# Kernel optimization log

Hardware: AMD Instinct MI355X
Metric: run time of the kernel (lower is better)

## Reference

```python
import jax, jax.numpy as jnp
import numpy as np

N = 100000   # nodes
E = 1600000  # edges (avg degree 16)
G = 1024     # graphs in batch
F = 128      # node feature dim
H = 128      # hidden channels


def setup_inputs() -> dict:
    key = jax.random.key(0)
    ks = jax.random.split(key, 12)
    s = 1.0 / np.sqrt(H)
    x = jax.random.normal(ks[0], (N, F), dtype=jnp.float32)
    edge_index = jax.random.randint(ks[1], (2, E), 0, N, dtype=jnp.int32)
    batch = jnp.sort(jax.random.randint(ks[2], (N,), 0, G, dtype=jnp.int32))
    return {
        "x": x,
        "edge_index": edge_index,
        "batch": batch,
        "W1": jax.random.normal(ks[3], (F, H), dtype=jnp.float32) * s,
        "b1": jnp.zeros((H,), jnp.float32),
        "W2": jax.random.normal(ks[4], (H, H), dtype=jnp.float32) * s,
        "b2": jnp.zeros((H,), jnp.float32),
        "W3": jax.random.normal(ks[5], (H, H), dtype=jnp.float32) * s,
        "b3": jnp.zeros((H,), jnp.float32),
        "W4": jax.random.normal(ks[6], (H, H), dtype=jnp.float32) * s,
        "b4": jnp.zeros((H,), jnp.float32),
        "linW": jax.random.normal(ks[7], (H, 2), dtype=jnp.float32) * s,
        "linb": jnp.zeros((2,), jnp.float32),
    }


def _gcn_conv(h, W, b, src, dst, norm, n):
    # h' = D^{-1/2}(A+I)D^{-1/2} (h W) + b   (PyG GCNConv default)
    m = h @ W                              # [n, H]
    msg = m[src] * norm[:, None]           # [E+n, H] gather + scale
    out = jax.ops.segment_sum(msg, dst, num_segments=n)
    return out + b


def reference(x, edge_index, batch, W1, b1, W2, b2, W3, b3, W4, b4, linW, linb):
    n = x.shape[0]
    loops = jnp.arange(n, dtype=edge_index.dtype)
    src = jnp.concatenate([edge_index[0], loops])   # add self-loops
    dst = jnp.concatenate([edge_index[1], loops])
    deg = jax.ops.segment_sum(jnp.ones_like(dst, dtype=x.dtype), dst, num_segments=n)
    dinv = jax.lax.rsqrt(deg)                       # deg >= 1 due to self-loops
    norm = dinv[src] * dinv[dst]                    # [E+n]

    h = jax.nn.relu(_gcn_conv(x, W1, b1, src, dst, norm, n))
    h = jax.nn.relu(_gcn_conv(h, W2, b2, src, dst, norm, n))
    h = jax.nn.relu(_gcn_conv(h, W3, b3, src, dst, norm, n))
    h = jax.nn.relu(_gcn_conv(h, W4, b4, src, dst, norm, n))

    # global_mean_pool over `batch` segment ids
    counts = jax.ops.segment_sum(jnp.ones((n,), x.dtype), batch, num_segments=G)
    pooled = jax.ops.segment_sum(h, batch, num_segments=G) / jnp.maximum(counts, 1.0)[:, None]

    # dropout p=0.5 is identity in eval mode
    return pooled @ linW + linb
```

## Files before the change

kernel.cpp:

```cpp
#include <hip/hip_runtime.h>
#include <math.h>

#define NF 128
#define NU 64
#define NQ 32
#define TROWS 32
#define ARS 68
#define CRS 132
#define QS  16.0f
#define QIS 0.0625f

#define SRC_BITS 18
#define SRC_MASK ((1u << SRC_BITS) - 1u)
#define BCS 32
#define EPB 2048

typedef unsigned int  u32;
typedef unsigned short u16;
typedef u32 b4 __attribute__((ext_vector_type(2)));
typedef short bf16x8 __attribute__((ext_vector_type(8)));
typedef float f32x4 __attribute__((ext_vector_type(4)));
typedef float f32x2 __attribute__((ext_vector_type(2)));

__device__ inline u16 f2bf(float f) {
    u32 u = __float_as_uint(f);
    return (u16)((u + 0x7fffu + ((u >> 16) & 1u)) >> 16);
}
__device__ inline u32 pack2(float a, float b) {
    return (u32)f2bf(a) | ((u32)f2bf(b) << 16);
}
__device__ inline float bflo(u32 u) { return __uint_as_float(u << 16); }
__device__ inline float bfhi(u32 u) { return __uint_as_float(u & 0xffff0000u); }

__device__ inline u32 pack4(float a, float b, float c, float d) {
    u32 v = __builtin_amdgcn_cvt_pk_fp8_f32(a, b, 0, false);
    v = __builtin_amdgcn_cvt_pk_fp8_f32(c, d, v, true);
    return v;
}
__device__ inline void acc4(float4& a, u32 q) {
    f32x2 lo = __builtin_amdgcn_cvt_pk_f32_fp8(q, false);
    f32x2 hi = __builtin_amdgcn_cvt_pk_f32_fp8(q, true);
    a.x += lo[0]; a.y += lo[1]; a.z += hi[0]; a.w += hi[1];
}


__global__ __launch_bounds__(256) void k_bscat(const int* __restrict__ ei,
                                               int* bcur, u32* __restrict__ pairs,
                                               int E, int bshift, int cap) {
    __shared__ int h[256];
    __shared__ int rb[256];
    int t = threadIdx.x;
    h[t] = 0;
    __syncthreads();
    int base = blockIdx.x * EPB;
    #pragma unroll
    for (int k = 0; k < EPB / 256; ++k) {
        int e = base + k * 256 + t;
        if (e < E) atomicAdd(&h[ei[E + e] >> bshift], 1);
    }
    __syncthreads();
    int c = h[t];
    if (c) rb[t] = t * cap + atomicAdd(&bcur[t * BCS], c);
    h[t] = 0;
    __syncthreads();
    #pragma unroll
    for (int k = 0; k < EPB / 256; ++k) {
        int e = base + k * 256 + t;
        if (e < E) {
            int d = ei[E + e];
            int b = d >> bshift;
            int p = rb[b] + atomicAdd(&h[b], 1);
            u32 rel = (u32)(d - (b << bshift));
            pairs[p] = (rel << SRC_BITS) | (u32)ei[e];
        }
    }
}

__global__ __launch_bounds__(512) void k_degscan(const u32* __restrict__ pairs,
        const int* __restrict__ bcur, float* __restrict__ dinv,
        int* __restrict__ offs, int* __restrict__ bsum,
        int n, int bshift, int cap) {
    extern __shared__ int sh[];
    int bsz = 1 << bshift;
    int* deg = sh;
    int* ss = sh + bsz;
    int b = blockIdx.x, b0 = b << bshift, t = threadIdx.x;
    for (int i = t; i < bsz; i += 512) deg[i] = 0;
    __syncthreads();
    int lo = b * cap, hi = lo + bcur[b * BCS];
    for (int j = lo + t; j < hi; j += 512)
        atomicAdd(&deg[pairs[j] >> SRC_BITS], 1);
    __syncthreads();
    int C = bsz >> 9;
    int vloc[8];
    int tsum = 0;
    for (int c = 0; c < C; ++c) {
        int i = t * C + c;
        int node = b0 + i;
        int v = 0;
        if (node < n) {
            int real = deg[i] + 1;
            dinv[node] = 1.0f / sqrtf((float)real);
            v = (real + 3) & ~3;
        }
        vloc[c] = tsum;
        tsum += v;
    }
    ss[t] = tsum;
    for (int d = 1; d < 512; d <<= 1) {
        __syncthreads();
        int a = (t >= d) ? ss[t - d] : 0;
        __syncthreads();
        ss[t] += a;
    }
    __syncthreads();
    int tbase = ss[t] - tsum;
    for (int c = 0; c < C; ++c) {
        int node = b0 + t * C + c;
        if (node < n) offs[node] = tbase + vloc[c];
    }
    if (t == 511) bsum[b] = ss[511];
}

__global__ __launch_bounds__(512) void k_csr(const u32* __restrict__ pairs,
        const int* __restrict__ bcur, const int* __restrict__ bsum,
        int* __restrict__ offs, int* __restrict__ srcS,
        int n, int nbk, int bshift, int cap) {
    extern __shared__ int sh[];
    __shared__ int ss[512];
    int bsz = 1 << bshift;
    int* cur = sh;
    int* endv = sh + bsz;
    int b = blockIdx.x, b0 = b << bshift, t = threadIdx.x;

    int v = (t < nbk) ? bsum[t] : 0;
    ss[t] = v;
    for (int d = 1; d < 512; d <<= 1) {
        __syncthreads();
        int a = (t >= d) ? ss[t - d] : 0;
        __syncthreads();
        ss[t] += a;
    }
    __syncthreads();
    int bsumb = bsum[b];
    int base = ss[b] - bsumb;
    int nextbase = ss[b];
    int total = ss[511];
    if (b == nbk - 1 && t == 0) offs[n] = total;

    for (int i = t; i < bsz; i += 512) {
        int node = b0 + i;
        int o = 0;
        if (node < n) {
            o = offs[node] + base;
            offs[node] = o;
        }
        cur[i] = o;
    }
    __syncthreads();
    for (int i = t; i < bsz; i += 512) {
        int node = b0 + i;
        int e;
        if (node + 1 >= n)       e = total;
        else if (i < bsz - 1)    e = cur[i + 1];
        else                     e = nextbase;
        endv[i] = e;
    }
    __syncthreads();
    int lo = b * cap, hi = lo + bcur[b * BCS];
    for (int j = lo + t; j < hi; j += 512) {
        u32 vv = pairs[j];
        int p = atomicAdd(&cur[vv >> SRC_BITS], 1);
        srcS[p] = (int)(vv & SRC_MASK);
    }
    __syncthreads();
    for (int i = t; i < bsz; i += 512) {
        int node = b0 + i;
        if (node < n) {
            int c = cur[i];
            srcS[c] = node;
            int e = endv[i];
            for (int k = c + 1; k < e; ++k) srcS[k] = n;
        }
    }
}

__global__ __launch_bounds__(256) void k_pack(const float* __restrict__ x,
                       const float* __restrict__ dinv, u32* __restrict__ q,
                       const float* __restrict__ W0, const float* __restrict__ W1,
                       const float* __restrict__ W2, const float* __restrict__ W3,
                       u32* __restrict__ wt, int n) {
    int t = blockIdx.x * blockDim.x + threadIdx.x;
    int totalu4 = (n + 1) * (NQ / 4);
    if (t < totalu4) {
        int row = t >> 3;
        uint4 o = make_uint4(0, 0, 0, 0);
        if (row < n) {
            int cbase = (t & 7) << 4;
            const float* xr = x + (size_t)row * NF + cbase;
            f32x4 f0 = __builtin_nontemporal_load((const f32x4*)(xr));
            f32x4 f1 = __builtin_nontemporal_load((const f32x4*)(xr + 4));
            f32x4 f2 = __builtin_nontemporal_load((const f32x4*)(xr + 8));
            f32x4 f3 = __builtin_nontemporal_load((const f32x4*)(xr + 12));
            float d = dinv[row] * QS;
            o.x = pack4(f0.x * d, f0.y * d, f0.z * d, f0.w * d);
            o.y = pack4(f1.x * d, f1.y * d, f1.z * d, f1.w * d);
            o.z = pack4(f2.x * d, f2.y * d, f2.z * d, f2.w * d);
            o.w = pack4(f3.x * d, f3.y * d, f3.z * d, f3.w * d);
        }
        ((uint4*)q)[t] = o;
    }
    if (t < 4 * 2048) {
        int layer = t >> 11;
        int rem = t & 2047;
        int lane = rem & 63;
        int ks = (rem >> 6) & 3;
        int nt = rem >> 8;
        const float* W = layer == 0 ? W0 : layer == 1 ? W1 : layer == 2 ? W2 : W3;
        int nn = nt * 16 + (lane & 15);
        int k0 = ks * 32 + (lane >> 4) * 8;
        uint4 o;
        o.x = pack2(W[(k0 + 0) * NF + nn], W[(k0 + 1) * NF + nn]);
        o.y = pack2(W[(k0 + 2) * NF + nn], W[(k0 + 3) * NF + nn]);
        o.z = pack2(W[(k0 + 4) * NF + nn], W[(k0 + 5) * NF + nn]);
        o.w = pack2(W[(k0 + 6) * NF + nn], W[(k0 + 7) * NF + nn]);
        ((uint4*)wt)[t] = o;
    }
}

__global__ __launch_bounds__(256, 8) void k_fused(
        const u32* __restrict__ hin, const int* __restrict__ offs,
        const int* __restrict__ srcS, const float* __restrict__ dinv,
        const u32* __restrict__ wt, const float* __restrict__ bias,
        u32* __restrict__ out, int* tctr, int n, int ntiles, int last) {
    __shared__ __align__(16) u32 buf[TROWS * CRS];
    __shared__ int stile;
    float* Cs = (float*)buf;
    int tid = threadIdx.x;
    int grp = tid >> 5;
    int lane32 = tid & 31;
    int c4 = lane32 << 2;
    int cu = lane32 << 1;
    int cq = lane32;
    int wv = tid >> 6;
    int lane = tid & 63;
    int m0 = (wv & 1) * 16;
    int nh = wv >> 1;
    int mrow = lane & 15, quad = lane >> 4;

    float4 bv = *(const float4*)(bias + c4);

    for (;;) {
        if (tid == 0) stile = atomicAdd(tctr, 1);
        __syncthreads();
        int tile = stile;
        if (tile >= ntiles) break;
        int row0 = tile * TROWS;

        #pragma unroll
        for (int i = 0; i < 4; ++i) {
            int r = grp * 4 + i;
            int node = row0 + r;
            float4 acc = make_float4(0.f, 0.f, 0.f, 0.f);
            if (node < n) {
                int b = offs[node], e = offs[node + 1];
                int j = b;
                for (; j + 8 <= e; j += 8) {
                    int4 sa = *(const int4*)(srcS + j);
                    int4 sb = *(const int4*)(srcS + j + 4);
                    u32 q0 = hin[(size_t)sa.x * NQ + cq];
                    u32 q1 = hin[(size_t)sa.y * NQ + cq];
                    u32 q2 = hin[(size_t)sa.z * NQ + cq];
                    u32 q3 = hin[(size_t)sa.w * NQ + cq];
                    u32 q4 = hin[(size_t)sb.x * NQ + cq];
                    u32 q5 = hin[(size_t)sb.y * NQ + cq];
                    u32 q6 = hin[(size_t)sb.z * NQ + cq];
                    u32 q7 = hin[(size_t)sb.w * NQ + cq];
                    acc4(acc, q0); acc4(acc, q1); acc4(acc, q2); acc4(acc, q3);
                    acc4(acc, q4); acc4(acc, q5); acc4(acc, q6); acc4(acc, q7);
                }
                if (j < e) {
                    int4 sa = *(const int4*)(srcS + j);
                    u32 q0 = hin[(size_t)sa.x * NQ + cq];
                    u32 q1 = hin[(size_t)sa.y * NQ + cq];
                    u32 q2 = hin[(size_t)sa.z * NQ + cq];
                    u32 q3 = hin[(size_t)sa.w * NQ + cq];
                    acc4(acc, q0); acc4(acc, q1); acc4(acc, q2); acc4(acc, q3);
                }
                float dn = dinv[node];
                acc.x *= dn; acc.y *= dn; acc.z *= dn; acc.w *= dn;
            }
            b4 o; o.x = pack2(acc.x, acc.y); o.y = pack2(acc.z, acc.w);
            *(b4*)(buf + r * ARS + cu) = o;
        }
        __syncthreads();

        f32x4 a0 = {0.f, 0.f, 0.f, 0.f}, a1 = a0, a2 = a0, a3 = a0;
        #pragma unroll
        for (int ks = 0; ks < 4; ++ks) {
            bf16x8 a = *(const bf16x8*)(buf + (m0 + mrow) * ARS + ks * 16 + quad * 4);
            const u32* wb = wt + (((nh * 4) * 4 + ks) * 64 + lane) * 4;
            bf16x8 b0 = *(const bf16x8*)(wb);
            bf16x8 b1 = *(const bf16x8*)(wb + 1024);
            bf16x8 b2 = *(const bf16x8*)(wb + 2048);
            bf16x8 b3 = *(const bf16x8*)(wb + 3072);
            a0 = __builtin_amdgcn_mfma_f32_16x16x32_bf16(a, b0, a0, 0, 0, 0);
            a1 = __builtin_amdgcn_mfma_f32_16x16x32_bf16(a, b1, a1, 0, 0, 0);
            a2 = __builtin_amdgcn_mfma_f32_16x16x32_bf16(a, b2, a2, 0, 0, 0);
            a3 = __builtin_amdgcn_mfma_f32_16x16x32_bf16(a, b3, a3, 0, 0, 0);
        }
        __syncthreads();

        #pragma unroll
        for (int nt = 0; nt < 4; ++nt) {
            f32x4 av = nt == 0 ? a0 : nt == 1 ? a1 : nt == 2 ? a2 : a3;
            int col = (nh * 4 + nt) * 16 + mrow;
            #pragma unroll
            for (int rg = 0; rg < 4; ++rg)
                Cs[(m0 + quad * 4 + rg) * CRS + col] = av[rg];
        }
        __syncthreads();

        #pragma unroll
        for (int j = 0; j < 4; ++j) {
            int r = grp * 4 + j;
            int gr = row0 + r;
            if (gr <= n) {
                if (last) {
                    b4 o; o.x = 0u; o.y = 0u;
                    if (gr < n) {
                        float4 v = *(const float4*)(Cs + r * CRS + c4);
                        float ox = fmaxf(v.x * QIS + bv.x, 0.f);
                        float oy = fmaxf(v.y * QIS + bv.y, 0.f);
                        float oz = fmaxf(v.z * QIS + bv.z, 0.f);
                        float ow = fmaxf(v.w * QIS + bv.w, 0.f);
                        o.x = pack2(ox, oy);
                        o.y = pack2(oz, ow);
                    }
                    *(b4*)(out + (size_t)gr * NU + cu) = o;
                } else {
                    u32 o = 0u;
                    if (gr < n) {
                        float4 v = *(const float4*)(Cs + r * CRS + c4);
                        float sc = dinv[gr] * QS;
                        float ox = fmaxf(v.x * QIS + bv.x, 0.f) * sc;
                        float oy = fmaxf(v.y * QIS + bv.y, 0.f) * sc;
                        float oz = fmaxf(v.z * QIS + bv.z, 0.f) * sc;
                        float ow = fmaxf(v.w * QIS + bv.w, 0.f) * sc;
                        o = pack4(ox, oy, oz, ow);
                    }
                    out[(size_t)gr * NQ + cq] = o;
                }
            }
        }
        __syncthreads();
    }
}


__global__ __launch_bounds__(256) void k_poolfinal(const u32* __restrict__ h,
        const int* __restrict__ batch, const float* __restrict__ linW,
        const float* __restrict__ linb, float* __restrict__ outp, int N) {
    int g = blockIdx.x;
    int tid = threadIdx.x;
    __shared__ int sb[2];
    if (tid < 2) {
        int target = g + tid;
        int lo = 0, hi = N;
        while (lo < hi) {
            int mid = (lo + hi) >> 1;
            if (batch[mid] < target) lo = mid + 1; else hi = mid;
        }
        sb[tid] = lo;
    }
    __syncthreads();
    int b = sb[0], e = sb[1];

    int grp = tid >> 5, lane = tid & 31;
    int c4 = lane << 2, cu = lane << 1;
    float4 acc = make_float4(0.f, 0.f, 0.f, 0.f);
    for (int i = b + grp; i < e; i += 8) {
        b4 v = *(const b4*)(h + (size_t)i * NU + cu);
        acc.x += bflo(v.x); acc.y += bfhi(v.x);
        acc.z += bflo(v.y); acc.w += bfhi(v.y);
    }
    __shared__ float red[8][NF];
    *(float4*)(&red[grp][c4]) = acc;
    __syncthreads();

    float v0 = 0.f, v1 = 0.f;
    if (tid < NF) {
        float s = 0.f;
        #pragma unroll
        for (int gg = 0; gg < 8; ++gg) s += red[gg][tid];
        v0 = s * linW[tid * 2 + 0];
        v1 = s * linW[tid * 2 + 1];
    }
    #pragma unroll
    for (int d = 32; d > 0; d >>= 1) {
        v0 += __shfl_down(v0, d);
        v1 += __shfl_down(v1, d);
    }
    __shared__ float sv[8];
    if ((tid & 63) == 0) { sv[(tid >> 6) * 2] = v0; sv[(tid >> 6) * 2 + 1] = v1; }
    __syncthreads();
    if (tid == 0) {
        float inv = 1.0f / fmaxf((float)(e - b), 1.0f);
        outp[g * 2 + 0] = (sv[0] + sv[2]) * inv + linb[0];
        outp[g * 2 + 1] = (sv[1] + sv[3]) * inv + linb[1];
    }
}


extern "C" void kernel_launch(void* const* d_in, const int* in_sizes, int n_in,
                              void* d_out, int out_size, void* d_ws, size_t ws_size,
                              hipStream_t stream) {
    const float* x     = (const float*)d_in[0];
    const int*   ei    = (const int*)d_in[1];
    const int*   batch = (const int*)d_in[2];
    const float* Wl[4] = {(const float*)d_in[3], (const float*)d_in[5],
                          (const float*)d_in[7], (const float*)d_in[9]};
    const float* bl[4] = {(const float*)d_in[4], (const float*)d_in[6],
                          (const float*)d_in[8], (const float*)d_in[10]};
    const float* linW  = (const float*)d_in[11];
    const float* linb  = (const float*)d_in[12];
    float* out = (float*)d_out;

    const int N  = in_sizes[2];
    const int E  = in_sizes[1] / 2;
    const int G  = out_size / 2;

    int bshift = 9;
    while (((N + (1 << bshift) - 1) >> bshift) > 256) ++bshift;
    int nbk = (N + (1 << bshift) - 1) >> bshift;
    int bsz = 1 << bshift;
    int cap = ((E / nbk) * 5 / 4 + 1024 + 255) & ~255;

    char* p = (char*)d_ws;
    auto carve = [&](size_t bytes) -> char* {
        char* r = p;
        p += (bytes + 255) & ~(size_t)255;
        return r;
    };
    float* dinv   = (float*)carve((size_t)N * 4);
    int*   offs   = (int*)  carve((size_t)(N + 1) * 4);
    int*   bsum   = (int*)  carve(512 * 4);
    int*   bcur   = (int*)  carve(256 * BCS * 4);
    int*   tctr   = (int*)  carve(4 * 4);
    u32*   wt     = (u32*)  carve(4 * 2048 * 16);
    int*   srcS   = (int*)  carve((size_t)(E + 4 * (size_t)N) * 4);
    u32*   bufA   = (u32*)  carve((size_t)(N + 1) * NU * 4);
    u32*   bufB   = (u32*)  carve((size_t)(N + 1) * NU * 4);
    u32*   pairs  = bufB;

    size_t zbytes = (char*)(tctr + 4) - (char*)bcur;
    (void)hipMemsetAsync(bcur, 0, zbytes, stream);

    int nblkE = (E + EPB - 1) / EPB;
    k_bscat<<<nblkE, 256, 0, stream>>>(ei, bcur, pairs, E, bshift, cap);
    k_degscan<<<nbk, 512, (bsz + 512) * 4, stream>>>(pairs, bcur, dinv, offs,
                                                     bsum, N, bshift, cap);
    k_csr<<<nbk, 512, 2 * bsz * 4, stream>>>(pairs, bcur, bsum, offs, srcS,
                                             N, nbk, bshift, cap);

    int totalu4 = (N + 1) * (NQ / 4);
    int packT = totalu4 > 8192 ? totalu4 : 8192;
    k_pack<<<(packT + 255) / 256, 256, 0, stream>>>(x, dinv, bufA,
                                                    Wl[0], Wl[1], Wl[2], Wl[3], wt, N);

    int ntiles = (N + 1 + TROWS - 1) / TROWS;
    int ngrid = ntiles < 2048 ? ntiles : 2048;
    const u32* hin = bufA;
    u32* hout = bufB;
    for (int l = 0; l < 4; ++l) {
        k_fused<<<ngrid, 256, 0, stream>>>(hin, offs, srcS, dinv, wt + l * 8192,
                                           bl[l], hout, tctr + l, N, ntiles, l == 3);
        hin = hout;
        hout = (hout == bufA) ? bufB : bufA;
    }

    k_poolfinal<<<G, 256, 0, stream>>>(hin, batch, linW, linb, out, N);
}
```

Baseline: 538.0 us.

## Partition each node's CSR neighbors into four source-range slices for gather locality

Each destination node's neighbor list is split into four segments by source-node range, each padded to a multiple of four. The fused layer kernel walks all tiles' nodes slice by slice, with a block barrier between slices, so concurrent blocks gather from a narrower part of the feature array and hit cache more often. The cost is extra padding entries (up to four pads per node), a bigger offset table, more shared memory and work in the CSR build, and extra barriers in the gather loop.

```diff
diff --git a/kernel.cpp b/kernel.cpp
--- a/kernel.cpp
+++ b/kernel.cpp
@@ -14,6 +14,7 @@
 #define SRC_MASK ((1u << SRC_BITS) - 1u)
 #define BCS 32
 #define EPB 2048
+#define NSL 4
 
 typedef unsigned int  u32;
 typedef unsigned short u16;
@@ -78,33 +79,42 @@
 
 __global__ __launch_bounds__(512) void k_degscan(const u32* __restrict__ pairs,
         const int* __restrict__ bcur, float* __restrict__ dinv,
-        int* __restrict__ offs, int* __restrict__ bsum,
-        int n, int bshift, int cap) {
+        int* __restrict__ offs, int* __restrict__ offsS4, int* __restrict__ bsum,
+        int n, int bshift, int cap, int slw) {
     extern __shared__ int sh[];
     int bsz = 1 << bshift;
     int* deg = sh;
-    int* ss = sh + bsz;
+    int* ss = sh + bsz * 4;
     int b = blockIdx.x, b0 = b << bshift, t = threadIdx.x;
-    for (int i = t; i < bsz; i += 512) deg[i] = 0;
+    for (int i = t; i < bsz * 4; i += 512) deg[i] = 0;
     __syncthreads();
     int lo = b * cap, hi = lo + bcur[b * BCS];
-    for (int j = lo + t; j < hi; j += 512)
-        atomicAdd(&deg[pairs[j] >> SRC_BITS], 1);
+    for (int j = lo + t; j < hi; j += 512) {
+        u32 v = pairs[j];
+        int rel = v >> SRC_BITS;
+        int src = (int)(v & SRC_MASK);
+        int s = src / slw; if (s > 3) s = 3;
+        atomicAdd(&deg[rel * 4 + s], 1);
+    }
     __syncthreads();
     int C = bsz >> 9;
-    int vloc[8];
+    int vst[8];
     int tsum = 0;
     for (int c = 0; c < C; ++c) {
         int i = t * C + c;
         int node = b0 + i;
-        int v = 0;
+        vst[c] = tsum;
         if (node < n) {
-            int real = deg[i] + 1;
+            int ssl = node / slw; if (ssl > 3) ssl = 3;
+            int real = 1;
+            #pragma unroll
+            for (int s = 0; s < 4; ++s) {
+                int cc = deg[i * 4 + s] + (s == ssl ? 1 : 0);
+                real += deg[i * 4 + s];
+                tsum += (cc + 3) & ~3;
+            }
             dinv[node] = 1.0f / sqrtf((float)real);
-            v = (real + 3) & ~3;
-        }
-        vloc[c] = tsum;
-        tsum += v;
+        }
     }
     ss[t] = tsum;
     for (int d = 1; d < 512; d <<= 1) {
@@ -116,21 +126,32 @@
     __syncthreads();
     int tbase = ss[t] - tsum;
     for (int c = 0; c < C; ++c) {
-        int node = b0 + t * C + c;
-        if (node < n) offs[node] = tbase + vloc[c];
+        int i = t * C + c;
+        int node = b0 + i;
+        if (node < n) {
+            int pos = tbase + vst[c];
+            offs[node] = pos;
+            int ssl = node / slw; if (ssl > 3) ssl = 3;
+            #pragma unroll
+            for (int s = 0; s < 4; ++s) {
+                offsS4[node * 4 + s] = pos;
+                int cc = deg[i * 4 + s] + (s == ssl ? 1 : 0);
+                pos += (cc + 3) & ~3;
+            }
+        }
     }
     if (t == 511) bsum[b] = ss[511];
 }
 
 __global__ __launch_bounds__(512) void k_csr(const u32* __restrict__ pairs,
         const int* __restrict__ bcur, const int* __restrict__ bsum,
-        int* __restrict__ offs, int* __restrict__ srcS,
-        int n, int nbk, int bshift, int cap) {
+        int* __restrict__ offs, int* __restrict__ offsS4, int* __restrict__ srcS,
+        int n, int nbk, int bshift, int cap, int slw) {
     extern __shared__ int sh[];
     __shared__ int ss[512];
     int bsz = 1 << bshift;
     int* cur = sh;
-    int* endv = sh + bsz;
+    int* endv = sh + bsz * 4;
     int b = blockIdx.x, b0 = b << bshift, t = threadIdx.x;
 
     int v = (t < nbk) ? bsum[t] : 0;
@@ -142,45 +163,62 @@
         ss[t] += a;
     }
     __syncthreads();
-    int bsumb = bsum[b];
-    int base = ss[b] - bsumb;
+    int base = ss[b] - bsum[b];
     int nextbase = ss[b];
     int total = ss[511];
     if (b == nbk - 1 && t == 0) offs[n] = total;
 
     for (int i = t; i < bsz; i += 512) {
         int node = b0 + i;
-        int o = 0;
         if (node < n) {
-            o = offs[node] + base;
-            offs[node] = o;
-        }
-        cur[i] = o;
+            offs[node] += base;
+            int4 o4 = *(int4*)(offsS4 + node * 4);
+            o4.x += base; o4.y += base; o4.z += base; o4.w += base;
+            *(int4*)(offsS4 + node * 4) = o4;
+            cur[i * 4 + 0] = o4.x; cur[i * 4 + 1] = o4.y;
+            cur[i * 4 + 2] = o4.z; cur[i * 4 + 3] = o4.w;
+        } else {
+            cur[i * 4 + 0] = 0; cur[i * 4 + 1] = 0;
+            cur[i * 4 + 2] = 0; cur[i * 4 + 3] = 0;
+        }
     }
     __syncthreads();
     for (int i = t; i < bsz; i += 512) {
         int node = b0 + i;
-        int e;
-        if (node + 1 >= n)       e = total;
-        else if (i < bsz - 1)    e = cur[i + 1];
-        else                     e = nextbase;
-        endv[i] = e;
+        if (node < n) {
+            endv[i * 4 + 0] = cur[i * 4 + 1];
+            endv[i * 4 + 1] = cur[i * 4 + 2];
+            endv[i * 4 + 2] = cur[i * 4 + 3];
+            int e3;
+            if (node + 1 >= n)    e3 = total;
+            else if (i < bsz - 1) e3 = cur[(i + 1) * 4 + 0];
+            else                  e3 = nextbase;
+            endv[i * 4 + 3] = e3;
+        }
     }
     __syncthreads();
     int lo = b * cap, hi = lo + bcur[b * BCS];
     for (int j = lo + t; j < hi; j += 512) {
         u32 vv = pairs[j];
-        int p = atomicAdd(&cur[vv >> SRC_BITS], 1);
-        srcS[p] = (int)(vv & SRC_MASK);
+        int rel = vv >> SRC_BITS;
+        int src = (int)(vv & SRC_MASK);
+        int s = src / slw; if (s > 3) s = 3;
+        int p = atomicAdd(&cur[rel * 4 + s], 1);
+        srcS[p] = src;
     }
     __syncthreads();
     for (int i = t; i < bsz; i += 512) {
         int node = b0 + i;
         if (node < n) {
-            int c = cur[i];
-            srcS[c] = node;
-            int e = endv[i];
-            for (int k = c + 1; k < e; ++k) srcS[k] = n;
+            int ssl = node / slw; if (ssl > 3) ssl = 3;
+            int p = cur[i * 4 + ssl]++;
+            srcS[p] = node;
+            #pragma unroll
+            for (int s = 0; s < 4; ++s) {
+                int c = cur[i * 4 + s];
+                int e = endv[i * 4 + s];
+                for (int k = c; k < e; ++k) srcS[k] = n;
+            }
         }
     }
 }
@@ -230,9 +268,10 @@
 
 __global__ __launch_bounds__(256, 8) void k_fused(
         const u32* __restrict__ hin, const int* __restrict__ offs,
-        const int* __restrict__ srcS, const float* __restrict__ dinv,
-        const u32* __restrict__ wt, const float* __restrict__ bias,
-        u32* __restrict__ out, int* tctr, int n, int ntiles, int last) {
+        const int* __restrict__ offsS4, const int* __restrict__ srcS,
+        const float* __restrict__ dinv, const u32* __restrict__ wt,
+        const float* __restrict__ bias, u32* __restrict__ out,
+        int* tctr, int n, int ntiles, int last) {
     __shared__ __align__(16) u32 buf[TROWS * CRS];
     __shared__ int stile;
     float* Cs = (float*)buf;
@@ -257,40 +296,58 @@
         if (tile >= ntiles) break;
         int row0 = tile * TROWS;
 
+        float4 acc[4];
+        #pragma unroll
+        for (int i = 0; i < 4; ++i) acc[i] = make_float4(0.f, 0.f, 0.f, 0.f);
+        #pragma unroll
+        for (int s = 0; s < NSL; ++s) {
+            #pragma unroll
+            for (int i = 0; i < 4; ++i) {
+                int node = row0 + grp * 4 + i;
+                if (node < n) {
+                    int b = offsS4[node * 4 + s];
+                    int e = (s < NSL - 1) ? offsS4[node * 4 + s + 1]
+                                          : offs[node + 1];
+                    int j = b;
+                    for (; j + 8 <= e; j += 8) {
+                        int4 sa = *(const int4*)(srcS + j);
+                        int4 sb = *(const int4*)(srcS + j + 4);
+                        u32 q0 = hin[(size_t)sa.x * NQ + cq];
+                        u32 q1 = hin[(size_t)sa.y * NQ + cq];
+                        u32 q2 = hin[(size_t)sa.z * NQ + cq];
+                        u32 q3 = hin[(size_t)sa.w * NQ + cq];
+                        u32 q4 = hin[(size_t)sb.x * NQ + cq];
+                        u32 q5 = hin[(size_t)sb.y * NQ + cq];
+                        u32 q6 = hin[(size_t)sb.z * NQ + cq];
+                        u32 q7 = hin[(size_t)sb.w * NQ + cq];
+                        acc4(acc[i], q0); acc4(acc[i], q1);
+                        acc4(acc[i], q2); acc4(acc[i], q3);
+                        acc4(acc[i], q4); acc4(acc[i], q5);
+                        acc4(acc[i], q6); acc4(acc[i], q7);
+                    }
+                    if (j < e) {
+                        int4 sa = *(const int4*)(srcS + j);
+                        u32 q0 = hin[(size_t)sa.x * NQ + cq];
+                        u32 q1 = hin[(size_t)sa.y * NQ + cq];
+                        u32 q2 = hin[(size_t)sa.z * NQ + cq];
+                        u32 q3 = hin[(size_t)sa.w * NQ + cq];
+                        acc4(acc[i], q0); acc4(acc[i], q1);
+                        acc4(acc[i], q2); acc4(acc[i], q3);
+                    }
+                }
+            }
+            __syncthreads();
+        }
         #pragma unroll
         for (int i = 0; i < 4; ++i) {
             int r = grp * 4 + i;
             int node = row0 + r;
-            float4 acc = make_float4(0.f, 0.f, 0.f, 0.f);
+            float4 a = acc[i];
             if (node < n) {
-                int b = offs[node], e = offs[node + 1];
-                int j = b;
-                for (; j + 8 <= e; j += 8) {
-                    int4 sa = *(const int4*)(srcS + j);
-                    int4 sb = *(const int4*)(srcS + j + 4);
-                    u32 q0 = hin[(size_t)sa.x * NQ + cq];
-                    u32 q1 = hin[(size_t)sa.y * NQ + cq];
-                    u32 q2 = hin[(size_t)sa.z * NQ + cq];
-                    u32 q3 = hin[(size_t)sa.w * NQ + cq];
-                    u32 q4 = hin[(size_t)sb.x * NQ + cq];
-                    u32 q5 = hin[(size_t)sb.y * NQ + cq];
-                    u32 q6 = hin[(size_t)sb.z * NQ + cq];
-                    u32 q7 = hin[(size_t)sb.w * NQ + cq];
-                    acc4(acc, q0); acc4(acc, q1); acc4(acc, q2); acc4(acc, q3);
-                    acc4(acc, q4); acc4(acc, q5); acc4(acc, q6); acc4(acc, q7);
-                }
-                if (j < e) {
-                    int4 sa = *(const int4*)(srcS + j);
-                    u32 q0 = hin[(size_t)sa.x * NQ + cq];
-                    u32 q1 = hin[(size_t)sa.y * NQ + cq];
-                    u32 q2 = hin[(size_t)sa.z * NQ + cq];
-                    u32 q3 = hin[(size_t)sa.w * NQ + cq];
-                    acc4(acc, q0); acc4(acc, q1); acc4(acc, q2); acc4(acc, q3);
-                }
                 float dn = dinv[node];
-                acc.x *= dn; acc.y *= dn; acc.z *= dn; acc.w *= dn;
+                a.x *= dn; a.y *= dn; a.z *= dn; a.w *= dn;
             }
-            b4 o; o.x = pack2(acc.x, acc.y); o.y = pack2(acc.z, acc.w);
+            b4 o; o.x = pack2(a.x, a.y); o.y = pack2(a.z, a.w);
             *(b4*)(buf + r * ARS + cu) = o;
         }
         __syncthreads();
@@ -435,6 +492,7 @@
     int nbk = (N + (1 << bshift) - 1) >> bshift;
     int bsz = 1 << bshift;
     int cap = ((E / nbk) * 5 / 4 + 1024 + 255) & ~255;
+    int slw = (N + NSL - 1) / NSL;
 
     char* p = (char*)d_ws;
     auto carve = [&](size_t bytes) -> char* {
@@ -444,11 +502,12 @@
     };
     float* dinv   = (float*)carve((size_t)N * 4);
     int*   offs   = (int*)  carve((size_t)(N + 1) * 4);
+    int*   offsS4 = (int*)  carve((size_t)N * 4 * 4);
     int*   bsum   = (int*)  carve(512 * 4);
     int*   bcur   = (int*)  carve(256 * BCS * 4);
     int*   tctr   = (int*)  carve(4 * 4);
     u32*   wt     = (u32*)  carve(4 * 2048 * 16);
-    int*   srcS   = (int*)  carve((size_t)(E + 4 * (size_t)N) * 4);
+    int*   srcS   = (int*)  carve((size_t)(E + 20 * (size_t)N) * 4);
     u32*   bufA   = (u32*)  carve((size_t)(N + 1) * NU * 4);
     u32*   bufB   = (u32*)  carve((size_t)(N + 1) * NU * 4);
     u32*   pairs  = bufB;
@@ -458,10 +517,11 @@
 
     int nblkE = (E + EPB - 1) / EPB;
     k_bscat<<<nblkE, 256, 0, stream>>>(ei, bcur, pairs, E, bshift, cap);
-    k_degscan<<<nbk, 512, (bsz + 512) * 4, stream>>>(pairs, bcur, dinv, offs,
-                                                     bsum, N, bshift, cap);
-    k_csr<<<nbk, 512, 2 * bsz * 4, stream>>>(pairs, bcur, bsum, offs, srcS,
-                                             N, nbk, bshift, cap);
+    k_degscan<<<nbk, 512, (bsz * 4 + 512) * 4, stream>>>(pairs, bcur, dinv, offs,
+                                                         offsS4, bsum, N, bshift,
+                                                         cap, slw);
+    k_csr<<<nbk, 512, bsz * 8 * 4, stream>>>(pairs, bcur, bsum, offs, offsS4,
+                                             srcS, N, nbk, bshift, cap, slw);
 
     int totalu4 = (N + 1) * (NQ / 4);
     int packT = totalu4 > 8192 ? totalu4 : 8192;
@@ -473,8 +533,9 @@
     const u32* hin = bufA;
     u32* hout = bufB;
     for (int l = 0; l < 4; ++l) {
-        k_fused<<<ngrid, 256, 0, stream>>>(hin, offs, srcS, dinv, wt + l * 8192,
-                                           bl[l], hout, tctr + l, N, ntiles, l == 3);
+        k_fused<<<ngrid, 256, 0, stream>>>(hin, offs, offsS4, srcS, dinv,
+                                           wt + l * 8192, bl[l], hout,
+                                           tctr + l, N, ntiles, l == 3);
         hin = hout;
         hout = (hout == bufA) ? bufB : bufA;
     }
```

Measured after the change: 680.4 us. 26.5% more time.
